# Kernel tuning notes

Hardware: AMD Instinct MI355X
Metric: run time of the kernel (lower is better)

## Reference

```python
import jax, jax.numpy as jnp
import numpy as np


def _lsa(cost):
    """Jonker-Volgenant shortest-augmenting-path linear sum assignment.
    cost: [n, n] numpy float64, rows = ground_truth, cols = prediction.
    Returns col_of_row: col_of_row[i] = column assigned to row i.
    Matches scipy.optimize.linear_sum_assignment on square matrices."""
    n = cost.shape[0]
    INF = np.inf
    u = np.zeros(n + 1)
    v = np.zeros(n + 1)
    p = np.zeros(n + 1, dtype=np.int64)   # p[j] = row matched to column j (1-indexed, 0 = none)
    way = np.zeros(n + 1, dtype=np.int64)
    for i in range(1, n + 1):
        p[0] = i
        j0 = 0
        minv = np.full(n + 1, INF)
        used = np.zeros(n + 1, dtype=bool)
        while True:
            used[j0] = True
            i0 = p[j0]
            free = ~used[1:]
            cur = cost[i0 - 1, :] - u[i0] - v[1:]
            upd = free & (cur < minv[1:])
            minv1 = minv[1:]
            way1 = way[1:]
            minv1[upd] = cur[upd]
            way1[upd] = j0
            masked = np.where(free, minv1, INF)
            j1 = int(np.argmin(masked)) + 1
            delta = masked[j1 - 1]
            u[p[used]] += delta
            v[used] -= delta
            minv[1:][free] -= delta
            j0 = j1
            if p[j0] == 0:
                break
        while True:
            j1 = way[j0]
            p[j0] = p[j1]
            j0 = j1
            if j0 == 0:
                break
    col_of_row = np.zeros(n, dtype=np.int64)
    for j in range(1, n + 1):
        col_of_row[p[j] - 1] = j - 1
    return col_of_row


def _hungarian_perms(pred_np, target_np):
    """Per-batch L1 cost matrices (rows=target, cols=pred) + assignment.
    Returns perms [B, N]: perms[b, i] = pred index matched to target point i."""
    # [B, N, N] L1 cdist, computed in float64 on host (faithful to scipy CPU path)
    cost = np.abs(target_np[:, :, None, :].astype(np.float64)
                  - pred_np[:, None, :, :].astype(np.float64)).sum(-1)
    return np.stack([_lsa(c) for c in cost], axis=0)


def setup_inputs() -> dict:
    key = jax.random.key(0)
    k1, k2 = jax.random.split(key)
    B, N = 128, 64
    pred = jax.random.uniform(k1, (B, N, 2), dtype=jnp.float32)
    target = jax.random.uniform(k2, (B, N, 2), dtype=jnp.float32)
    return {"pred": pred, "target": target}


def reference(pred, target):
    # Host-side Hungarian matching (mirrors the scipy CPU round-trip; indices
    # are data-dependent and non-differentiable, exactly as in the original).
    pred_np = np.asarray(jax.device_get(pred))
    target_np = np.asarray(jax.device_get(target))
    perms = jnp.asarray(_hungarian_perms(pred_np, target_np))  # [B, N] int

    # Gather matched predictions: pred_sorted[b, i] = pred[b, perms[b, i]]
    pred_sorted = jnp.take_along_axis(pred, perms[:, :, None], axis=1)
    # Per-batch F.l1_loss is a mean over N*2 elements; summing over batch and
    # dividing by B equals the global mean (all batch elements same size).
    return jnp.mean(jnp.abs(pred_sorted - target))
```

## Files before the change

### kernel.cpp

```cpp
#include <hip/hip_runtime.h>

#define BATCH 128
#define NPTS  64

template<int CTRL>
__device__ __forceinline__ int dpp_mov_i(int x) {
    return __builtin_amdgcn_update_dpp(x, x, CTRL, 0xF, 0xF, false);
}

__global__ __launch_bounds__(64) void hungarian_kernel(
    const float* __restrict__ pred,
    const float* __restrict__ target,
    double* __restrict__ batch_cost)
{
    const int b    = blockIdx.x;
    const int lane = threadIdx.x;

    const float2 pr = ((const float2*)pred)[b * NPTS + lane];
    const float2 tg = ((const float2*)target)[b * NPTS + lane];
    const int pxi = (int)(pr.x * 8388608.0f);
    const int pyi = (int)(pr.y * 8388608.0f);
    const int txi = (int)(tg.x * 8388608.0f);
    const int tyi = (int)(tg.y * 8388608.0f);

    int vi = 0;
    int wi = 0;
    int p  = 0;

    for (int i = 1; i <= NPTS; ++i) {
        int  r     = i - 1;
        int  u0    = 0;
        int  D     = 0;
        int  Dsnap = 0;
        bool sel   = false;
        int  jf    = 0;

        for (;;) {
            int tx  = __builtin_amdgcn_readlane(txi, r);
            int ty  = __builtin_amdgcn_readlane(tyi, r);
            int dx  = tx - pxi; dx = (dx < 0) ? -dx : dx;
            int dy  = ty - pyi; dy = (dy < 0) ? -dy : dy;
            int cur = (dx + dy) - (u0 + vi);
            int key = sel ? 0x7FFFFFFF : cur;

            int m = key;
            m = min(m, dpp_mov_i<0x111>(m));
            m = min(m, dpp_mov_i<0x112>(m));
            m = min(m, dpp_mov_i<0x114>(m));
            m = min(m, dpp_mov_i<0x118>(m));
            int m0 = __builtin_amdgcn_readlane(m, 15);
            int m1 = __builtin_amdgcn_readlane(m, 31);
            int m2 = __builtin_amdgcn_readlane(m, 47);
            int m3 = __builtin_amdgcn_readlane(m, 63);
            int gmin = min(min(m0, m1), min(m2, m3));

            unsigned long long msk = __ballot(key == gmin);
            int j = __ffsll(msk) - 1;

            D += gmin;
            bool me = (lane == j);
            if (me) Dsnap = D;

            int pj = __builtin_amdgcn_readlane(p, j);
            if (pj == 0) { jf = j; break; }

            sel = sel || me;
            r   = pj - 1;
            u0  = __builtin_amdgcn_readlane(wi, j);
        }

        int S = D - Dsnap;
        if (sel) { wi += S; vi -= S; }
        if (lane == jf) { p = i; wi = D; }
    }

    int tpx = __shfl(txi, p - 1);
    int tpy = __shfl(tyi, p - 1);
    int dxf = tpx - pxi; dxf = (dxf < 0) ? -dxf : dxf;
    int dyf = tpy - pyi; dyf = (dyf < 0) ? -dyf : dyf;
    int ci = dxf + dyf;
    #pragma unroll
    for (int s = 32; s >= 1; s >>= 1) ci += __shfl_xor(ci, s);
    if (lane == 0) batch_cost[b] = (double)ci * 0x1p-23;
}

__global__ __launch_bounds__(64) void reduce_kernel(
    const double* __restrict__ batch_cost,
    float* __restrict__ out)
{
    int t = threadIdx.x;
    double x = batch_cost[t] + batch_cost[t + 64];
    #pragma unroll
    for (int s = 32; s >= 1; s >>= 1) x += __shfl_xor(x, s);
    if (t == 0) out[0] = (float)(x / (double)(BATCH * NPTS * 2));
}

extern "C" void kernel_launch(void* const* d_in, const int* in_sizes, int n_in,
                              void* d_out, int out_size, void* d_ws, size_t ws_size,
                              hipStream_t stream)
{
    const float* pred   = (const float*)d_in[0];
    const float* target = (const float*)d_in[1];
    double* batch_cost  = (double*)d_ws;

    hungarian_kernel<<<BATCH, 64, 0, stream>>>(pred, target, batch_cost);
    reduce_kernel<<<1, 64, 0, stream>>>(batch_cost, (float*)d_out);
}
```

Baseline: 62.66 us.

## Restructure Hungarian inner loop with per-column matched coords and freemask

```diff
diff --git a/kernel.cpp b/kernel.cpp
--- a/kernel.cpp
+++ b/kernel.cpp
@@ -6,6 +6,12 @@
 template<int CTRL>
 __device__ __forceinline__ int dpp_mov_i(int x) {
     return __builtin_amdgcn_update_dpp(x, x, CTRL, 0xF, 0xF, false);
+}
+
+__device__ __forceinline__ int imin(int a, int b) { return a < b ? a : b; }
+
+__device__ __forceinline__ unsigned sadu(unsigned a, unsigned b, unsigned c) {
+    return (a > b ? a - b : b - a) + c;
 }
 
 __global__ __launch_bounds__(64) void hungarian_kernel(
@@ -23,62 +29,60 @@
     const int txi = (int)(tg.x * 8388608.0f);
     const int tyi = (int)(tg.y * 8388608.0f);
 
-    int vi = 0;
-    int wi = 0;
-    int p  = 0;
+    int vi  = 0;
+    int cu  = 0;
+    int ctx = 0, cty = 0;
+    int pvx = pxi;
+    unsigned long long freemask = ~0ull;
 
-    for (int i = 1; i <= NPTS; ++i) {
-        int  r     = i - 1;
-        int  u0    = 0;
-        int  D     = 0;
-        int  Dsnap = 0;
-        bool sel   = false;
-        int  jf    = 0;
+    for (int i = 0; i < NPTS; ++i) {
+        const int rix = __builtin_amdgcn_readlane(txi, i);
+        const int riy = __builtin_amdgcn_readlane(tyi, i);
+        int key = (int)sadu((unsigned)rix, (unsigned)pvx,
+                            sadu((unsigned)riy, (unsigned)pyi, 0u)) - vi;
+        int  D = 0, Dsnap = 0, u0 = 0;
+        bool sel = false;
+        int  jf;
 
         for (;;) {
-            int tx  = __builtin_amdgcn_readlane(txi, r);
-            int ty  = __builtin_amdgcn_readlane(tyi, r);
-            int dx  = tx - pxi; dx = (dx < 0) ? -dx : dx;
-            int dy  = ty - pyi; dy = (dy < 0) ? -dy : dy;
-            int cur = (dx + dy) - (u0 + vi);
-            int key = sel ? 0x7FFFFFFF : cur;
-
-            int m = key;
-            m = min(m, dpp_mov_i<0x111>(m));
-            m = min(m, dpp_mov_i<0x112>(m));
-            m = min(m, dpp_mov_i<0x114>(m));
-            m = min(m, dpp_mov_i<0x118>(m));
-            int m0 = __builtin_amdgcn_readlane(m, 15);
-            int m1 = __builtin_amdgcn_readlane(m, 31);
-            int m2 = __builtin_amdgcn_readlane(m, 47);
-            int m3 = __builtin_amdgcn_readlane(m, 63);
-            int gmin = min(min(m0, m1), min(m2, m3));
-
-            unsigned long long msk = __ballot(key == gmin);
+            int m  = key;
+            int a1 = dpp_mov_i<0x111>(m);
+            int a2 = dpp_mov_i<0x112>(m);
+            m = imin(imin(m, a1), a2);
+            a1 = dpp_mov_i<0x113>(m);
+            a2 = dpp_mov_i<0x116>(m);
+            m = imin(imin(m, a1), a2);
+            a1 = dpp_mov_i<0x117>(m);
+            m = imin(m, a1);
+            int g = imin(imin(__builtin_amdgcn_readlane(m, 15),
+                              __builtin_amdgcn_readlane(m, 31)),
+                         imin(__builtin_amdgcn_readlane(m, 47),
+                              __builtin_amdgcn_readlane(m, 63)));
+            unsigned long long msk = __ballot(key == g);
             int j = __ffsll(msk) - 1;
 
-            D += gmin;
+            D += g - u0;
             bool me = (lane == j);
             if (me) Dsnap = D;
 
-            int pj = __builtin_amdgcn_readlane(p, j);
-            if (pj == 0) { jf = j; break; }
+            if (freemask & (1ull << j)) { jf = j; break; }
 
-            sel = sel || me;
-            r   = pj - 1;
-            u0  = __builtin_amdgcn_readlane(wi, j);
+            if (me) { pvx = 0x40000000; sel = true; }
+            u0 = __builtin_amdgcn_readlane(cu, j);
+            int ox = __builtin_amdgcn_readlane(ctx, j);
+            int oy = __builtin_amdgcn_readlane(cty, j);
+            key = (int)sadu((unsigned)ox, (unsigned)pvx,
+                            sadu((unsigned)oy, (unsigned)pyi, 0u)) - vi;
         }
 
         int S = D - Dsnap;
-        if (sel) { wi += S; vi -= S; }
-        if (lane == jf) { p = i; wi = D; }
+        if (sel) { cu += S; vi -= S; pvx = pxi; }
+        if (lane == jf) { ctx = rix; cty = riy; cu = D; }
+        freemask &= ~(1ull << jf);
     }
 
-    int tpx = __shfl(txi, p - 1);
-    int tpy = __shfl(tyi, p - 1);
-    int dxf = tpx - pxi; dxf = (dxf < 0) ? -dxf : dxf;
-    int dyf = tpy - pyi; dyf = (dyf < 0) ? -dyf : dyf;
-    int ci = dxf + dyf;
+    int ci = (int)sadu((unsigned)ctx, (unsigned)pxi,
+                       sadu((unsigned)cty, (unsigned)pyi, 0u));
     #pragma unroll
     for (int s = 32; s >= 1; s >>= 1) ci += __shfl_xor(ci, s);
     if (lane == 0) batch_cost[b] = (double)ci * 0x1p-23;
```

Result: faster. 59.45 us (-5.1%).
